# Optimization experiments

Hardware: AMD Instinct MI355X
Metric: run time of the kernel (lower is better)

Reference implementation:

```python
import jax, jax.numpy as jnp
import numpy as np

E = 8          # num experts
H = 1024       # hidden size
I = 512        # moe intermediate size
K = 2          # top_k
B, S = 1, 2048


def setup_inputs() -> dict:
    key = jax.random.key(0)
    k1, k2, k3, k4, k5 = jax.random.split(key, 5)
    hidden_states = jax.random.normal(k1, (B, S, H), dtype=jnp.float32)
    router_indices = jax.random.randint(k2, (B * S, K), 0, E, dtype=jnp.int64)
    routing_weights = jax.random.uniform(k3, (B * S, K), dtype=jnp.float32)
    # kaiming-uniform-ish init per expert
    bound_gu = 1.0 / np.sqrt(H)
    bound_d = 1.0 / np.sqrt(I)
    gate_up_proj = jax.random.uniform(k4, (E, H, 2 * I), dtype=jnp.float32,
                                      minval=-bound_gu, maxval=bound_gu)
    down_proj = jax.random.uniform(k5, (E, I, H), dtype=jnp.float32,
                                   minval=-bound_d, maxval=bound_d)
    return {
        "hidden_states": hidden_states,
        "router_indices": router_indices,
        "routing_weights": routing_weights,
        "gate_up_proj": gate_up_proj,
        "down_proj": down_proj,
    }


def reference(hidden_states, router_indices, routing_weights, gate_up_proj, down_proj):
    b, s, h = hidden_states.shape
    x = hidden_states.reshape(b * s, h)                    # [T, H]
    # combine weights: sum over top-k slots of routing weight for each expert
    one_hot = jax.nn.one_hot(router_indices, E, dtype=x.dtype)   # [T, K, E]
    combine = jnp.einsum('tke,tk->te', one_hot, routing_weights)  # [T, E]
    # dense dispatch: every token through every expert, masked/weighted by combine
    gate_up = jnp.einsum('th,ehf->tef', x, gate_up_proj)   # [T, E, 2I]
    gate, up = jnp.split(gate_up, 2, axis=-1)              # [T, E, I] each
    inter = jax.nn.silu(gate) * up                         # SwiGLU (no limit clamp)
    out = jnp.einsum('tef,efh,te->th', inter, down_proj, combine)  # [T, H]
    return out.reshape(b, s, h)
```

## Files before the change

kernel.cpp:

```cpp
#include <hip/hip_runtime.h>
#include <stdint.h>

#define T_TOK 2048
#define H_DIM 1024
#define ID    512
#define E_NUM 8
#define NPAIR 4096
#define BM    64
#define MAXTILES 72

typedef _Float16 half_t;
typedef _Float16 f16x8 __attribute__((ext_vector_type(8)));
typedef _Float16 f16x4 __attribute__((ext_vector_type(4)));
typedef float    f32x4 __attribute__((ext_vector_type(4)));

#define XB_OFF      ((size_t)0)
#define WGU_OFF     ((size_t)(4u << 20))
#define WDN_OFF     ((size_t)(20u << 20))
#define INTER_OFF   ((size_t)(28u << 20))
#define META_OFF    ((size_t)(32u << 20))
#define PAIRW_OFF   ((size_t)((32u << 20) + 65536))
#define CONTRIB_OFF ((size_t)(36u << 20))

__device__ __forceinline__ void gload_lds16(const void* g, void* l) {
    __builtin_amdgcn_global_load_lds(
        (const __attribute__((address_space(1))) unsigned int*)g,
        (__attribute__((address_space(3))) unsigned int*)l,
        16, 0, 0);
}

template <int NT>
__device__ __forceinline__ void cvt_tile64(const float* __restrict__ in,
                                           half_t* __restrict__ out,
                                           int r0, int c0, int out_stride,
                                           char* smem) {
    float (*tile)[65] = (float(*)[65])smem;
    int tid = threadIdx.x;
#pragma unroll
    for (int it = 0; it < 1024 / NT; it++) {
        int idx = tid + it * NT;
        int r = idx >> 4, c4 = (idx & 15) * 4;
        float4 v = *(const float4*)(in + (size_t)(r0 + r) * 1024 + c0 + c4);
        tile[r][c4] = v.x; tile[r][c4 + 1] = v.y; tile[r][c4 + 2] = v.z; tile[r][c4 + 3] = v.w;
    }
    __syncthreads();
#pragma unroll
    for (int it = 0; it < 1024 / NT; it++) {
        int idx = tid + it * NT;
        int oc = idx >> 4, r4 = (idx & 15) * 4;
        f16x4 o;
        o[0] = (half_t)tile[r4][oc];
        o[1] = (half_t)tile[r4 + 1][oc];
        o[2] = (half_t)tile[r4 + 2][oc];
        o[3] = (half_t)tile[r4 + 3][oc];
        *(f16x4*)(out + (size_t)(c0 + oc) * out_stride + r0 + r4) = o;
    }
}

__global__ __launch_bounds__(256) void k_prep(const float* __restrict__ x,
                                              const int* __restrict__ ridx,
                                              const float* __restrict__ rw,
                                              const float* __restrict__ wgu,
                                              half_t* __restrict__ xb,
                                              half_t* __restrict__ wguT,
                                              int* __restrict__ meta,
                                              float* __restrict__ pair_w) {
    __shared__ char smem[16704];
    int b = blockIdx.x, tid = threadIdx.x;
    if (b < 1024) {
        int g = b * 256 + tid;
        size_t b0 = (size_t)g * 8;
        float4 v0 = *(const float4*)(x + b0);
        float4 v1 = *(const float4*)(x + b0 + 4);
        f16x8 o;
        o[0] = (half_t)v0.x; o[1] = (half_t)v0.y; o[2] = (half_t)v0.z; o[3] = (half_t)v0.w;
        o[4] = (half_t)v1.x; o[5] = (half_t)v1.y; o[6] = (half_t)v1.z; o[7] = (half_t)v1.w;
        *(f16x8*)(xb + b0) = o;
    } else if (b == 1024) {
        __shared__ int cnt[E_NUM], cur[E_NUM], base[E_NUM];
        if (tid < E_NUM) { cnt[tid] = 0; cur[tid] = 0; }
        __syncthreads();
        for (int i = tid; i < NPAIR; i += 256) atomicAdd(&cnt[ridx[i]], 1);
        __syncthreads();
        if (tid == 0) {
            int acc = 0, nt = 0;
            for (int e = 0; e < E_NUM; e++) {
                base[e] = acc;
                for (int r = 0; r < cnt[e]; r += BM) {
                    meta[8 + nt] = e; meta[88 + nt] = acc + r; meta[168 + nt] = acc + cnt[e]; nt++;
                }
                acc += cnt[e];
            }
            meta[0] = nt;
        }
        __syncthreads();
        for (int i = tid; i < NPAIR; i += 256) {
            int e = ridx[i];
            int pos = atomicAdd(&cur[e], 1);
            int slot = base[e] + pos;
            meta[256 + slot] = i >> 1;
            meta[256 + NPAIR + i] = slot;
            pair_w[slot] = rw[i];
        }
    } else {
        int t = b - 1025;
        int e = t >> 8, rem = t & 255;
        int h0 = (rem >> 4) * 64, f0 = (rem & 15) * 64;
        cvt_tile64<256>(wgu + (size_t)e * 1024 * 1024, wguT + (size_t)e * 1024 * 1024,
                        h0, f0, 1024, smem);
    }
}

template <int MODE>
__global__ __launch_bounds__(256) void k_gemm(const int* __restrict__ meta,
                                              const half_t* __restrict__ amat,
                                              const half_t* __restrict__ wT,
                                              const float* __restrict__ pair_w,
                                              void* __restrict__ outp,
                                              const float* __restrict__ aux_in,
                                              half_t* __restrict__ aux_out) {
    constexpr int KSZ = MODE ? ID : H_DIM;
    constexpr int NKT = KSZ / 64;
    __shared__ __align__(16) char smem[49152];

    int d = blockIdx.x;
    if (MODE == 0 && d >= 576) {
        int d2 = d - 576;
        int e = d2 >> 7, rem = d2 & 127;
        int h0 = (rem >> 3) * 64, i0 = (rem & 7) * 64;
        cvt_tile64<256>(aux_in + (size_t)e * ID * 1024, aux_out + (size_t)e * 1024 * ID,
                        i0, h0, ID, smem);
        return;
    }

    int l = (d & 7) * MAXTILES + (d >> 3);
    int bx = l >> 3, by = l & 7;
    int nt = meta[0];
    if (bx >= nt) return;
    int e = meta[8 + bx], row0 = meta[88 + bx], rend = meta[168 + bx];
    const int* pair_token = meta + 256;

    int tid = threadIdx.x, lane = tid & 63, wid = tid >> 6;

    const half_t* asrc[2]; int aoff[2];
#pragma unroll
    for (int i = 0; i < 2; i++) {
        int gch = wid * 2 + i, c = gch * 64 + lane;
        int r = c >> 3, pc = c & 7, lc = pc ^ (r & 7);
        int pr = row0 + r; if (pr > NPAIR - 1) pr = NPAIR - 1;
        const half_t* rowp = (MODE == 0) ? amat + (size_t)pair_token[pr] * KSZ
                                         : amat + (size_t)pr * KSZ;
        asrc[i] = rowp + lc * 8;
        aoff[i] = gch * 1024 + lane * 16;
    }
    const half_t* wbase = wT + (size_t)e * 1024 * KSZ;
    const half_t* bsrc[4]; int boff[4];
#pragma unroll
    for (int i = 0; i < 4; i++) {
        int gch = wid * 4 + i, c = gch * 64 + lane;
        int r = c >> 3, pc = c & 7, lc = pc ^ (r & 7);
        int physcol;
        if (MODE == 0) {
            int wn_r = r >> 5, fn_r = (r >> 4) & 1, ll = r & 15;
            physcol = by * 64 + wn_r * 16 + ll + (fn_r ? 512 : 0);
        } else {
            physcol = by * 128 + r;
        }
        bsrc[i] = wbase + (size_t)physcol * KSZ + lc * 8;
        boff[i] = gch * 1024 + lane * 16;
    }

#define STAGE(buf, kt)                                                             \
    {                                                                              \
        _Pragma("unroll")                                                          \
        for (int i = 0; i < 2; i++)                                                \
            gload_lds16(asrc[i] + (kt) * 64, smem + (buf) * 8192 + aoff[i]);       \
        _Pragma("unroll")                                                          \
        for (int i = 0; i < 4; i++)                                                \
            gload_lds16(bsrc[i] + (kt) * 64, smem + 16384 + (buf) * 16384 + boff[i]); \
    }

    f32x4 acc[4][2] = {};

    STAGE(0, 0);
    __syncthreads();

    for (int kt = 0; kt < NKT; kt++) {
        int cur = kt & 1;
        if (kt + 1 < NKT) STAGE(cur ^ 1, kt + 1);
        const char* Ab = smem + cur * 8192;
        const char* Bb = smem + 16384 + cur * 16384;
#pragma unroll
        for (int ks = 0; ks < 2; ks++) {
            f16x8 af[4], bf2[2];
#pragma unroll
            for (int f = 0; f < 4; f++) {
                int ar = f * 16 + (lane & 15);
                int apc = (ks * 4 + (lane >> 4)) ^ (ar & 7);
                af[f] = *(const f16x8*)(Ab + ar * 128 + apc * 16);
            }
#pragma unroll
            for (int f = 0; f < 2; f++) {
                int br = wid * 32 + f * 16 + (lane & 15);
                int bpc = (ks * 4 + (lane >> 4)) ^ (br & 7);
                bf2[f] = *(const f16x8*)(Bb + br * 128 + bpc * 16);
            }
#pragma unroll
            for (int fm = 0; fm < 4; fm++)
#pragma unroll
                for (int fn = 0; fn < 2; fn++)
                    acc[fm][fn] = __builtin_amdgcn_mfma_f32_16x16x32_f16(af[fm], bf2[fn], acc[fm][fn], 0, 0, 0);
        }
        __syncthreads();
    }

    if (MODE == 0) {
        half_t* inter = (half_t*)outp;
#pragma unroll
        for (int fm = 0; fm < 4; fm++) {
            int rbase = fm * 16 + (lane >> 4) * 4;
#pragma unroll
            for (int j = 0; j < 4; j++) {
                int packed = row0 + rbase + j;
                if (packed < rend) {
                    float gv = acc[fm][0][j], uv = acc[fm][1][j];
                    float s = gv / (1.0f + __expf(-gv)) * uv;
                    int col = by * 64 + wid * 16 + (lane & 15);
                    inter[(size_t)packed * ID + col] = (half_t)s;
                }
            }
        }
    } else {
        float* contrib = (float*)outp;
#pragma unroll
        for (int fm = 0; fm < 4; fm++) {
            int rbase = fm * 16 + (lane >> 4) * 4;
#pragma unroll
            for (int j = 0; j < 4; j++) {
                int packed = row0 + rbase + j;
                if (packed < rend) {
                    float pw = pair_w[packed];
#pragma unroll
                    for (int fn = 0; fn < 2; fn++) {
                        int col = by * 128 + wid * 32 + fn * 16 + (lane & 15);
                        contrib[(size_t)packed * H_DIM + col] = acc[fm][fn][j] * pw;
                    }
                }
            }
        }
    }
#undef STAGE
}

__global__ __launch_bounds__(256) void k_gather(const float* __restrict__ contrib,
                                                const int* __restrict__ meta,
                                                float* __restrict__ out) {
    int t = blockIdx.x, c4 = threadIdx.x * 4;
    const int* slot_of = meta + 256 + NPAIR;
    int s0 = slot_of[2 * t], s1 = slot_of[2 * t + 1];
    float4 a = *(const float4*)(contrib + (size_t)s0 * H_DIM + c4);
    float4 b = *(const float4*)(contrib + (size_t)s1 * H_DIM + c4);
    float4 o;
    o.x = a.x + b.x; o.y = a.y + b.y; o.z = a.z + b.z; o.w = a.w + b.w;
    *(float4*)(out + (size_t)t * H_DIM + c4) = o;
}

extern "C" void kernel_launch(void* const* d_in, const int* in_sizes, int n_in,
                              void* d_out, int out_size, void* d_ws, size_t ws_size,
                              hipStream_t stream) {
    const float* x    = (const float*)d_in[0];
    const int*   ridx = (const int*)d_in[1];
    const float* rw   = (const float*)d_in[2];
    const float* wgu  = (const float*)d_in[3];
    const float* wdn  = (const float*)d_in[4];
    float* out = (float*)d_out;

    char* ws = (char*)d_ws;
    half_t* xb      = (half_t*)(ws + XB_OFF);
    half_t* wguT    = (half_t*)(ws + WGU_OFF);
    half_t* wdnT    = (half_t*)(ws + WDN_OFF);
    half_t* inter   = (half_t*)(ws + INTER_OFF);
    int*    meta    = (int*)(ws + META_OFF);
    float*  pair_w  = (float*)(ws + PAIRW_OFF);
    float*  contrib = (float*)(ws + CONTRIB_OFF);

    k_prep<<<3073, 256, 0, stream>>>(x, ridx, rw, wgu, xb, wguT, meta, pair_w);
    k_gemm<0><<<1600, 256, 0, stream>>>(meta, xb, wguT, pair_w, inter, wdn, wdnT);
    k_gemm<1><<<576, 256, 0, stream>>>(meta, inter, wdnT, pair_w, contrib, nullptr, nullptr);
    k_gather<<<T_TOK, 256, 0, stream>>>(contrib, meta, out);
}
```

Measured before the change: 61.54 us.

## Enlarge GEMM M-tile to 128 rows with a 2x2 warp layout

Doubles the row tile of both grouped GEMMs from 64 to 128 pairs. The four waves now form a 2x2 grid, and each wave computes a 64x64 output block with 16 accumulators. This is meant to raise MFMA work per LDS load and cut the number of tiles and redundant weight loads. In exchange it uses more LDS (64KB) and registers, launches fewer blocks (lower parallelism), and wastes more padding rows per expert.

```diff
diff --git a/kernel.cpp b/kernel.cpp
--- a/kernel.cpp
+++ b/kernel.cpp
@@ -6,8 +6,8 @@
 #define ID    512
 #define E_NUM 8
 #define NPAIR 4096
-#define BM    64
-#define MAXTILES 72
+#define BM    128
+#define MAXTILES 40
 
 typedef _Float16 half_t;
 typedef _Float16 f16x8 __attribute__((ext_vector_type(8)));
@@ -121,11 +121,11 @@
                                               half_t* __restrict__ aux_out) {
     constexpr int KSZ = MODE ? ID : H_DIM;
     constexpr int NKT = KSZ / 64;
-    __shared__ __align__(16) char smem[49152];
+    __shared__ __align__(16) char smem[65536];
 
     int d = blockIdx.x;
-    if (MODE == 0 && d >= 576) {
-        int d2 = d - 576;
+    if (MODE == 0 && d >= 320) {
+        int d2 = d - 320;
         int e = d2 >> 7, rem = d2 & 127;
         int h0 = (rem >> 3) * 64, i0 = (rem & 7) * 64;
         cvt_tile64<256>(aux_in + (size_t)e * ID * 1024, aux_out + (size_t)e * 1024 * ID,
@@ -141,12 +141,13 @@
     const int* pair_token = meta + 256;
 
     int tid = threadIdx.x, lane = tid & 63, wid = tid >> 6;
-
-    const half_t* asrc[2]; int aoff[2];
-#pragma unroll
-    for (int i = 0; i < 2; i++) {
-        int gch = wid * 2 + i, c = gch * 64 + lane;
-        int r = c >> 3, pc = c & 7, lc = pc ^ (r & 7);
+    int wm = wid >> 1, wn = wid & 1;
+
+    const half_t* asrc[4]; int aoff[4];
+#pragma unroll
+    for (int i = 0; i < 4; i++) {
+        int gch = wid * 4 + i;
+        int r = gch * 8 + (lane >> 3), pc = lane & 7, lc = pc ^ (r & 7);
         int pr = row0 + r; if (pr > NPAIR - 1) pr = NPAIR - 1;
         const half_t* rowp = (MODE == 0) ? amat + (size_t)pair_token[pr] * KSZ
                                          : amat + (size_t)pr * KSZ;
@@ -157,30 +158,30 @@
     const half_t* bsrc[4]; int boff[4];
 #pragma unroll
     for (int i = 0; i < 4; i++) {
-        int gch = wid * 4 + i, c = gch * 64 + lane;
-        int r = c >> 3, pc = c & 7, lc = pc ^ (r & 7);
+        int gch = wid * 4 + i;
+        int r = gch * 8 + (lane >> 3), pc = lane & 7, lc = pc ^ (r & 7);
         int physcol;
         if (MODE == 0) {
-            int wn_r = r >> 5, fn_r = (r >> 4) & 1, ll = r & 15;
-            physcol = by * 64 + wn_r * 16 + ll + (fn_r ? 512 : 0);
+            int wn_r = r >> 6, f_r = (r >> 4) & 3, ll = r & 15;
+            physcol = by * 64 + wn_r * 32 + (f_r & 1) * 16 + ll + ((f_r & 2) ? 512 : 0);
         } else {
             physcol = by * 128 + r;
         }
         bsrc[i] = wbase + (size_t)physcol * KSZ + lc * 8;
-        boff[i] = gch * 1024 + lane * 16;
+        boff[i] = 16384 + gch * 1024 + lane * 16;
     }
 
 #define STAGE(buf, kt)                                                             \
     {                                                                              \
         _Pragma("unroll")                                                          \
-        for (int i = 0; i < 2; i++)                                                \
-            gload_lds16(asrc[i] + (kt) * 64, smem + (buf) * 8192 + aoff[i]);       \
+        for (int i = 0; i < 4; i++)                                                \
+            gload_lds16(asrc[i] + (kt) * 64, smem + (buf) * 32768 + aoff[i]);      \
         _Pragma("unroll")                                                          \
         for (int i = 0; i < 4; i++)                                                \
-            gload_lds16(bsrc[i] + (kt) * 64, smem + 16384 + (buf) * 16384 + boff[i]); \
-    }
-
-    f32x4 acc[4][2] = {};
+            gload_lds16(bsrc[i] + (kt) * 64, smem + (buf) * 32768 + boff[i]);      \
+    }
+
+    f32x4 acc[4][4] = {};
 
     STAGE(0, 0);
     __syncthreads();
@@ -188,28 +189,25 @@
     for (int kt = 0; kt < NKT; kt++) {
         int cur = kt & 1;
         if (kt + 1 < NKT) STAGE(cur ^ 1, kt + 1);
-        const char* Ab = smem + cur * 8192;
-        const char* Bb = smem + 16384 + cur * 16384;
+        const char* Ab = smem + cur * 32768;
+        const char* Bb = Ab + 16384;
 #pragma unroll
         for (int ks = 0; ks < 2; ks++) {
-            f16x8 af[4], bf2[2];
+            f16x8 af[4], bf[4];
 #pragma unroll
             for (int f = 0; f < 4; f++) {
-                int ar = f * 16 + (lane & 15);
+                int ar = wm * 64 + f * 16 + (lane & 15);
                 int apc = (ks * 4 + (lane >> 4)) ^ (ar & 7);
                 af[f] = *(const f16x8*)(Ab + ar * 128 + apc * 16);
-            }
-#pragma unroll
-            for (int f = 0; f < 2; f++) {
-                int br = wid * 32 + f * 16 + (lane & 15);
+                int br = wn * 64 + f * 16 + (lane & 15);
                 int bpc = (ks * 4 + (lane >> 4)) ^ (br & 7);
-                bf2[f] = *(const f16x8*)(Bb + br * 128 + bpc * 16);
+                bf[f] = *(const f16x8*)(Bb + br * 128 + bpc * 16);
             }
 #pragma unroll
             for (int fm = 0; fm < 4; fm++)
 #pragma unroll
-                for (int fn = 0; fn < 2; fn++)
-                    acc[fm][fn] = __builtin_amdgcn_mfma_f32_16x16x32_f16(af[fm], bf2[fn], acc[fm][fn], 0, 0, 0);
+                for (int fn = 0; fn < 4; fn++)
+                    acc[fm][fn] = __builtin_amdgcn_mfma_f32_16x16x32_f16(af[fm], bf[fn], acc[fm][fn], 0, 0, 0);
         }
         __syncthreads();
     }
@@ -218,15 +216,18 @@
         half_t* inter = (half_t*)outp;
 #pragma unroll
         for (int fm = 0; fm < 4; fm++) {
-            int rbase = fm * 16 + (lane >> 4) * 4;
+            int rbase = wm * 64 + fm * 16 + (lane >> 4) * 4;
 #pragma unroll
             for (int j = 0; j < 4; j++) {
                 int packed = row0 + rbase + j;
                 if (packed < rend) {
-                    float gv = acc[fm][0][j], uv = acc[fm][1][j];
-                    float s = gv / (1.0f + __expf(-gv)) * uv;
-                    int col = by * 64 + wid * 16 + (lane & 15);
-                    inter[(size_t)packed * ID + col] = (half_t)s;
+                    half_t* rowp = inter + (size_t)packed * ID;
+#pragma unroll
+                    for (int fn = 0; fn < 2; fn++) {
+                        int col = by * 64 + wn * 32 + fn * 16 + (lane & 15);
+                        float g = acc[fm][fn][j], u = acc[fm][fn + 2][j];
+                        rowp[col] = (half_t)(g / (1.0f + __expf(-g)) * u);
+                    }
                 }
             }
         }
@@ -234,15 +235,15 @@
         float* contrib = (float*)outp;
 #pragma unroll
         for (int fm = 0; fm < 4; fm++) {
-            int rbase = fm * 16 + (lane >> 4) * 4;
+            int rbase = wm * 64 + fm * 16 + (lane >> 4) * 4;
 #pragma unroll
             for (int j = 0; j < 4; j++) {
                 int packed = row0 + rbase + j;
                 if (packed < rend) {
                     float pw = pair_w[packed];
 #pragma unroll
-                    for (int fn = 0; fn < 2; fn++) {
-                        int col = by * 128 + wid * 32 + fn * 16 + (lane & 15);
+                    for (int fn = 0; fn < 4; fn++) {
+                        int col = by * 128 + wn * 64 + fn * 16 + (lane & 15);
                         contrib[(size_t)packed * H_DIM + col] = acc[fm][fn][j] * pw;
                     }
                 }
@@ -285,7 +286,7 @@
     float*  contrib = (float*)(ws + CONTRIB_OFF);
 
     k_prep<<<3073, 256, 0, stream>>>(x, ridx, rw, wgu, xb, wguT, meta, pair_w);
-    k_gemm<0><<<1600, 256, 0, stream>>>(meta, xb, wguT, pair_w, inter, wdn, wdnT);
-    k_gemm<1><<<576, 256, 0, stream>>>(meta, inter, wdnT, pair_w, contrib, nullptr, nullptr);
+    k_gemm<0><<<1344, 256, 0, stream>>>(meta, xb, wguT, pair_w, inter, wdn, wdnT);
+    k_gemm<1><<<320, 256, 0, stream>>>(meta, inter, wdnT, pair_w, contrib, nullptr, nullptr);
     k_gather<<<T_TOK, 256, 0, stream>>>(contrib, meta, out);
 }
```

After: 64.98 us. 1.06x slower.
